# Kernel tuning notes

Measured on AMD Instinct MI355X. Metric: run time of the kernel, lower is better.

Reference implementation:

```python
import jax, jax.numpy as jnp
import numpy as np

WH, WW = 8, 8          # window_size
NUM_HEADS = 16
DIM = 512
NW = 64                # windows per image (mask leading dim)
BATCH = 16             # images
N = WH * WW            # tokens per window


def _relative_position_index():
    coords = np.stack(np.meshgrid(np.arange(WH), np.arange(WW), indexing='ij'))  # (2,Wh,Ww)
    cf = coords.reshape(2, -1)                                                   # (2,N)
    rel = cf[:, :, None] - cf[:, None, :]                                        # (2,N,N)
    rel = rel.transpose(1, 2, 0).astype(np.int64)                                # (N,N,2)
    rel[:, :, 0] += WH - 1
    rel[:, :, 1] += WW - 1
    rel[:, :, 0] *= 2 * WW - 1
    return jnp.asarray(rel.sum(-1), dtype=jnp.int32)                             # (N,N)


def setup_inputs() -> dict:
    key = jax.random.key(0)
    ks = jax.random.split(key, 8)
    B_ = BATCH * NW
    x = jax.random.normal(ks[0], (B_, N, DIM), dtype=jnp.float32)
    # 0 / -100 additive shift-style mask (Swin uses -100.0 for masked pairs)
    mraw = jax.random.uniform(ks[1], (NW, N, N))
    mask = jnp.where(mraw < 0.15, jnp.float32(-100.0), jnp.float32(0.0))
    qkv_w = jax.random.normal(ks[2], (3 * DIM, DIM), dtype=jnp.float32) * (DIM ** -0.5)
    qkv_b = jnp.zeros((3 * DIM,), dtype=jnp.float32)
    proj_w = jax.random.normal(ks[3], (DIM, DIM), dtype=jnp.float32) * (DIM ** -0.5)
    proj_b = jnp.zeros((DIM,), dtype=jnp.float32)
    n_rel = (2 * WH - 1) * (2 * WW - 1)  # 225
    rpb_table = jax.random.normal(ks[4], (n_rel, NUM_HEADS), dtype=jnp.float32) * 0.02
    rel_index = _relative_position_index()
    return {"x": x, "mask": mask, "qkv_w": qkv_w, "qkv_b": qkv_b,
            "proj_w": proj_w, "proj_b": proj_b, "rpb_table": rpb_table,
            "rel_index": rel_index}


def reference(x, mask, qkv_w, qkv_b, proj_w, proj_b, rpb_table, rel_index):
    B_, n, C = x.shape
    H = NUM_HEADS
    hd = C // H
    scale = hd ** -0.5
    qkv = x @ qkv_w.T + qkv_b                       # (B_, N, 3C)
    qkv = qkv.reshape(B_, n, 3, H, hd)
    q = qkv[:, :, 0].transpose(0, 2, 1, 3) * scale  # (B_, H, N, hd)
    k = qkv[:, :, 1].transpose(0, 2, 1, 3)
    v = qkv[:, :, 2].transpose(0, 2, 1, 3)
    attn = jnp.einsum('bhnd,bhmd->bhnm', q, k)      # (B_, H, N, N)
    bias = rpb_table[rel_index.reshape(-1)].reshape(n, n, H).transpose(2, 0, 1)  # (H,N,N)
    attn = attn + bias[None]
    nW = mask.shape[0]
    attn = attn.reshape(B_ // nW, nW, H, n, n) + mask[None, :, None]
    attn = jax.nn.softmax(attn.reshape(B_, H, n, n), axis=-1)
    out = jnp.einsum('bhnm,bhmd->bhnd', attn, v)    # (B_, H, N, hd)
    out = out.transpose(0, 2, 1, 3).reshape(B_, n, C)
    return out @ proj_w.T + proj_b
```

## Files before the change

### kernel.cpp

```cpp
#include <hip/hip_runtime.h>
#include <hip/hip_bf16.h>

typedef unsigned short u16;
typedef __attribute__((ext_vector_type(8))) short bfrag;
typedef __attribute__((ext_vector_type(4))) float ffrag;

#define NWIN_TOT 1024
#define NTOK 64
#define CDIM 512
#define NHEAD 16
#define HDIM 32
#define NW 64

__device__ __forceinline__ u16 f2bf(float f) {
  union { float f; unsigned u; } v; v.f = f;
  unsigned r = v.u + 0x7fffu + ((v.u >> 16) & 1u);
  return (u16)(r >> 16);
}

__device__ __forceinline__ float bfhi2f(unsigned hi_bits) {
  union { unsigned u; float f; } v; v.u = hi_bits; return v.f;
}

__device__ __forceinline__ ffrag mfma16(bfrag a, bfrag b, ffrag c) {
  return __builtin_amdgcn_mfma_f32_16x16x32_bf16(a, b, c, 0, 0, 0);
}

__device__ __forceinline__ void gload16(const u16* src, u16* lds) {
  __builtin_amdgcn_global_load_lds(
      (const __attribute__((address_space(1))) unsigned int*)src,
      (__attribute__((address_space(3))) unsigned int*)lds, 16, 0, 0);
}

#define BAR() __builtin_amdgcn_s_barrier()
#define VMW(n) do { asm volatile("s_waitcnt vmcnt(" #n ")" ::: "memory"); \
                    __builtin_amdgcn_sched_barrier(0); } while (0)

__global__ __launch_bounds__(256) void k_prep(const float* __restrict__ x,
                                              const float* __restrict__ qkv_w,
                                              const float* __restrict__ proj_w,
                                              const int*   __restrict__ rel_index,
                                              const float* __restrict__ rpb,
                                              const float* __restrict__ mask,
                                              u16* __restrict__ xb,
                                              u16* __restrict__ wq, u16* __restrict__ wp,
                                              u16* __restrict__ combB) {
  int i = blockIdx.x * 256 + threadIdx.x;
  if (i < 4194304) {
    int e = i * 8;
    const float4* xp = reinterpret_cast<const float4*>(x + e);
    float4 lo = xp[0], hi = xp[1];
    union { u16 u[8]; bfrag v; } pk;
    pk.u[0] = f2bf(lo.x); pk.u[1] = f2bf(lo.y); pk.u[2] = f2bf(lo.z); pk.u[3] = f2bf(lo.w);
    pk.u[4] = f2bf(hi.x); pk.u[5] = f2bf(hi.y); pk.u[6] = f2bf(hi.z); pk.u[7] = f2bf(hi.w);
    *reinterpret_cast<bfrag*>(xb + e) = pk.v;
    return;
  }
  i -= 4194304;
  if (i < 786432) { wq[i] = f2bf(qkv_w[i]); return; }
  i -= 786432;
  if (i < 262144) { wp[i] = f2bf(proj_w[i]); return; }
  i -= 262144;
  {
    int wh = i >> 12, rc = i & 4095;
    int w0 = wh >> 4, h = wh & 15;
    combB[i] = f2bf(rpb[rel_index[rc] * 16 + h] + mask[(w0 << 12) + rc]);
  }
}

template<int EPI>
__global__ __launch_bounds__(512, 1) void k_gemm3(const u16* __restrict__ A,
                                                  const u16* __restrict__ W,
                                                  const float* __restrict__ bias,
                                                  u16* __restrict__ qws, u16* __restrict__ kws,
                                                  u16* __restrict__ vws,
                                                  float* __restrict__ out) {
  constexpr int NT = (EPI == 0) ? 12 : 4;
  constexpr int NWG = 256 * NT;
  extern __shared__ __align__(16) u16 smem[];

  const int bid = blockIdx.x;
  const int tile = (bid & 7) * (NWG >> 3) + (bid >> 3);
  const int bn = tile % NT, bm = tile / NT;
  const int brow = bm << 8, bcol = bn << 7;

  const int tid = threadIdx.x;
  const int wv = tid >> 6, lane = tid & 63, c15 = lane & 15, g = lane >> 4;
  const int g4 = g * 4;
  const int wr = wv >> 1, wc = wv & 1;
  const ffrag zf = {0.f, 0.f, 0.f, 0.f};

  ffrag acc[4][4];
#pragma unroll
  for (int i = 0; i < 4; ++i)
#pragma unroll
    for (int n = 0; n < 4; ++n) acc[i][n] = zf;

  auto stageA = [&](int t) {
    u16* db = smem + (t % 3) * 24576;
#pragma unroll
    for (int l = 0; l < 4; ++l) {
      int e = l * 4096 + tid * 8;
      int r = e >> 6, cb = (e & 63) << 1;
      int scol = (cb ^ ((r & 7) << 4)) >> 1;
      gload16(A + (size_t)(brow + r) * 512 + t * 64 + scol, db + e);
    }
  };
  auto stageB = [&](int t) {
    u16* db = smem + (t % 3) * 24576 + 16384;
#pragma unroll
    for (int l = 0; l < 2; ++l) {
      int e = l * 4096 + tid * 8;
      int r = e >> 6, cb = (e & 63) << 1;
      int scol = (cb ^ ((r & 7) << 4)) >> 1;
      gload16(W + (size_t)(bcol + r) * 512 + t * 64 + scol, db + e);
    }
  };

  stageA(0); stageB(0); stageA(1); stageB(1);
  VMW(6);
  BAR();

  for (int t = 0; t < 8; ++t) {
    const char* As_ = (const char*)(smem + (t % 3) * 24576);
    const char* Bs_ = As_ + 32768;
    bfrag a_[4], b_[4];

#pragma unroll
    for (int i = 0; i < 4; ++i) {
      int ra = wr * 64 + i * 16 + c15;
      a_[i] = *(const bfrag*)(As_ + ra * 128 + ((g * 16) ^ ((ra & 7) << 4)));
    }
#pragma unroll
    for (int n = 0; n < 4; ++n) {
      int rb = wc * 64 + n * 16 + c15;
      b_[n] = *(const bfrag*)(Bs_ + rb * 128 + ((g * 16) ^ ((rb & 7) << 4)));
    }
    if (t + 2 < 8) stageA(t + 2);
    BAR();
    __builtin_amdgcn_s_setprio(1);
#pragma unroll
    for (int i = 0; i < 4; ++i)
#pragma unroll
      for (int n = 0; n < 4; ++n)
        acc[i][n] = mfma16(a_[i], b_[n], acc[i][n]);
    __builtin_amdgcn_s_setprio(0);

#pragma unroll
    for (int i = 0; i < 4; ++i) {
      int ra = wr * 64 + i * 16 + c15;
      a_[i] = *(const bfrag*)(As_ + ra * 128 + ((64 + g * 16) ^ ((ra & 7) << 4)));
    }
#pragma unroll
    for (int n = 0; n < 4; ++n) {
      int rb = wc * 64 + n * 16 + c15;
      b_[n] = *(const bfrag*)(Bs_ + rb * 128 + ((64 + g * 16) ^ ((rb & 7) << 4)));
    }
    if (t + 2 < 8) stageB(t + 2);
    __builtin_amdgcn_s_setprio(1);
#pragma unroll
    for (int i = 0; i < 4; ++i)
#pragma unroll
      for (int n = 0; n < 4; ++n)
        acc[i][n] = mfma16(a_[i], b_[n], acc[i][n]);
    __builtin_amdgcn_s_setprio(0);
    if (t < 6) { VMW(6); BAR(); }
    else if (t == 6) { VMW(0); BAR(); }
  }

  if (EPI == 0) {
    const float SCALE = 0.17677669529663687f;
    const int which = bn >> 2;
    const int win = (brow >> 6) + wr;
#pragma unroll
    for (int n = 0; n < 4; ++n) {
      int c = bcol + wc * 64 + n * 16 + c15;
      float bz = bias[c];
      int cq = c & 511, h = cq >> 5, d = cq & 31;
      size_t slab = ((size_t)(win * NHEAD + h)) << 11;
      if (which == 2) {
        u16* vp = vws + slab + (d << 6);
#pragma unroll
        for (int i = 0; i < 4; ++i) {
          int tok0 = i * 16 + g4;
          union { u16 u[4]; uint2 v; } pk;
#pragma unroll
          for (int r = 0; r < 4; ++r) pk.u[r] = f2bf(acc[i][n][r] + bz);
          *reinterpret_cast<uint2*>(vp + tok0) = pk.v;
        }
      } else {
        const float s = (which == 0) ? SCALE : 1.0f;
        u16* qp = ((which == 0) ? qws : kws) + slab + d;
#pragma unroll
        for (int i = 0; i < 4; ++i)
#pragma unroll
          for (int r = 0; r < 4; ++r)
            qp[(i * 16 + g4 + r) << 5] = f2bf((acc[i][n][r] + bz) * s);
      }
    }
  } else {
#pragma unroll
    for (int n = 0; n < 4; ++n) {
      int c = bcol + wc * 64 + n * 16 + c15;
      float bz = bias[c];
      float* po = out + (size_t)(brow + wr * 64) * CDIM + c;
#pragma unroll
      for (int i = 0; i < 4; ++i)
#pragma unroll
        for (int r = 0; r < 4; ++r)
          po[(size_t)(i * 16 + g4 + r) * CDIM] = acc[i][n][r] + bz;
    }
  }
}

__global__ __launch_bounds__(256) void k_attn(const u16* __restrict__ qws,
                                              const u16* __restrict__ kws,
                                              const u16* __restrict__ vws,
                                              const u16* __restrict__ combB,
                                              u16* __restrict__ yws) {
  __shared__ __align__(16) u16 plds[4][NTOK * NTOK];
  const int tid = threadIdx.x, w = tid >> 6, lane = tid & 63;
  const int c15 = lane & 15, g = lane >> 4, g4 = g * 4;
  const int p = blockIdx.x * 4 + w;
  const int b = p >> 4, h = p & 15;

  const u16* qb_ = qws + (size_t)p * (NTOK * HDIM);
  const u16* kb_ = kws + (size_t)p * (NTOK * HDIM);
  bfrag qa[4], ka[4];
#pragma unroll
  for (int t = 0; t < 4; ++t) {
    qa[t] = *reinterpret_cast<const bfrag*>(qb_ + (t * 16 + c15) * HDIM + g * 8);
    ka[t] = *reinterpret_cast<const bfrag*>(kb_ + (t * 16 + c15) * HDIM + g * 8);
  }

  const u16* cB = combB + ((size_t)(((b & (NW - 1)) << 4) + h) << 12);
  u16* pl = plds[w];
  const ffrag zf = {0.f, 0.f, 0.f, 0.f};

#pragma unroll
  for (int it = 0; it < 4; ++it) {
    int row = it * 16 + c15;
    float l[4][4];
    float mx = -3.0e38f;
#pragma unroll
    for (int jt = 0; jt < 4; ++jt) {
      ffrag s = mfma16(ka[jt], qa[it], zf);
      uint2 cw = *reinterpret_cast<const uint2*>(cB + row * 64 + jt * 16 + g4);
      l[jt][0] = s[0] + bfhi2f(cw.x << 16);
      l[jt][1] = s[1] + bfhi2f(cw.x & 0xffff0000u);
      l[jt][2] = s[2] + bfhi2f(cw.y << 16);
      l[jt][3] = s[3] + bfhi2f(cw.y & 0xffff0000u);
      mx = fmaxf(mx, fmaxf(fmaxf(l[jt][0], l[jt][1]), fmaxf(l[jt][2], l[jt][3])));
    }
    mx = fmaxf(mx, __shfl_xor(mx, 16));
    mx = fmaxf(mx, __shfl_xor(mx, 32));
    float sum = 0.f;
#pragma unroll
    for (int jt = 0; jt < 4; ++jt)
#pragma unroll
      for (int r = 0; r < 4; ++r) {
        float e = __expf(l[jt][r] - mx);
        l[jt][r] = e;
        sum += e;
      }
    sum += __shfl_xor(sum, 16);
    sum += __shfl_xor(sum, 32);
    float inv = 1.0f / sum;
#pragma unroll
    for (int jt = 0; jt < 4; ++jt) {
      union { u16 u[4]; uint2 v; } pk;
#pragma unroll
      for (int r = 0; r < 4; ++r) pk.u[r] = f2bf(l[jt][r] * inv);
      int off = row * 64 + ((jt * 16 + g4) ^ ((row & 7) << 3));
      *reinterpret_cast<uint2*>(&pl[off]) = pk.v;
    }
  }
  __syncthreads();

  const u16* vb_ = vws + (size_t)p * (HDIM * NTOK);
  ffrag o0[4] = {zf, zf, zf, zf}, o1[4] = {zf, zf, zf, zf};
#pragma unroll
  for (int ks = 0; ks < 2; ++ks) {
    bfrag vf0 = *reinterpret_cast<const bfrag*>(vb_ + c15 * NTOK + ks * 32 + g * 8);
    bfrag vf1 = *reinterpret_cast<const bfrag*>(vb_ + (16 + c15) * NTOK + ks * 32 + g * 8);
#pragma unroll
    for (int i = 0; i < 4; ++i) {
      int prow = i * 16 + c15;
      bfrag pa = *reinterpret_cast<const bfrag*>(
          &pl[prow * 64 + ((ks * 32 + g * 8) ^ ((prow & 7) << 3))]);
      o0[i] = mfma16(pa, vf0, o0[i]);
      o1[i] = mfma16(pa, vf1, o1[i]);
    }
  }
  __syncthreads();

  u16* yl = &plds[0][0];
#pragma unroll
  for (int i = 0; i < 4; ++i)
#pragma unroll
    for (int r = 0; r < 4; ++r) {
      int tok = i * 16 + g4 + r;
      yl[tok * 136 + w * 32 + c15] = f2bf(o0[i][r]);
      yl[tok * 136 + w * 32 + 16 + c15] = f2bf(o1[i][r]);
    }
  __syncthreads();
  {
    const int b2 = blockIdx.x >> 2;
    const int h0 = (blockIdx.x * 4) & 15;
    int row = tid >> 2, seg = tid & 3;
    const u16* src = yl + row * 136 + seg * 32;
    u16* dst = yws + ((size_t)b2 * NTOK + row) * CDIM + h0 * HDIM + seg * 32;
    bfrag v0 = *(const bfrag*)(src);
    bfrag v1 = *(const bfrag*)(src + 8);
    bfrag v2 = *(const bfrag*)(src + 16);
    bfrag v3 = *(const bfrag*)(src + 24);
    *(bfrag*)(dst) = v0;
    *(bfrag*)(dst + 8) = v1;
    *(bfrag*)(dst + 16) = v2;
    *(bfrag*)(dst + 24) = v3;
  }
}

extern "C" void kernel_launch(void* const* d_in, const int* in_sizes, int n_in,
                              void* d_out, int out_size, void* d_ws, size_t ws_size,
                              hipStream_t stream) {
  const float* x      = (const float*)d_in[0];
  const float* mask   = (const float*)d_in[1];
  const float* qkv_w  = (const float*)d_in[2];
  const float* qkv_b  = (const float*)d_in[3];
  const float* proj_w = (const float*)d_in[4];
  const float* proj_b = (const float*)d_in[5];
  const float* rpb    = (const float*)d_in[6];
  const int*   rel    = (const int*)d_in[7];
  float* out = (float*)d_out;

  char* ws = (char*)d_ws;
  constexpr size_t SZ_QKV = (size_t)NWIN_TOT * NHEAD * NTOK * HDIM * 2;
  u16* qws = (u16*)(ws);
  u16* kws = (u16*)(ws + SZ_QKV);
  u16* vws = (u16*)(ws + 2 * SZ_QKV);
  u16* xb  = (u16*)(ws + 3 * SZ_QKV);
  u16* yws = xb;
  u16* wq  = (u16*)(ws + 4 * SZ_QKV);
  u16* wp  = (u16*)(ws + 4 * SZ_QKV + 1572864);
  u16* combB = (u16*)(ws + 4 * SZ_QKV + 1572864 + 524288);

  hipFuncSetAttribute((const void*)k_gemm3<0>,
                      hipFuncAttributeMaxDynamicSharedMemorySize, 147456);
  hipFuncSetAttribute((const void*)k_gemm3<1>,
                      hipFuncAttributeMaxDynamicSharedMemorySize, 147456);

  k_prep<<<dim3(36864), dim3(256), 0, stream>>>(x, qkv_w, proj_w, rel, rpb, mask,
                                                xb, wq, wp, combB);
  k_gemm3<0><<<dim3(256 * 12), dim3(512), 147456, stream>>>(xb, wq, qkv_b,
                                                            qws, kws, vws, nullptr);
  k_attn<<<dim3(NWIN_TOT * NHEAD / 4), dim3(256), 0, stream>>>(qws, kws, vws, combB, yws);
  k_gemm3<1><<<dim3(256 * 4), dim3(512), 147456, stream>>>(yws, wp, proj_b,
                                                           nullptr, nullptr, nullptr, out);
}
```

Baseline: 324.5 us.

## Keep full 128-row A panel resident in LDS and stream weights from global

Restructures both GEMMs so each workgroup loads a 128x512 slab of activations into LDS once, then loops over all output column tiles, reading weight fragments straight from global memory (relying on cache) instead of staging them through LDS. The grid shrinks from thousands of 256x128 tiles to 512 row-panel workgroups, which removes the repeated re-reads of A across column tiles and the per-k-step barriers. In exchange it drops the triple-buffered software pipeline, uses a smaller per-wave accumulator tile, and makes the MFMA loop depend on global-load latency for W with no explicit prefetch.

New measurement: 417.3 us. 28.6% more time.

```diff
diff --git a/kernel.cpp b/kernel.cpp
--- a/kernel.cpp
+++ b/kernel.cpp
@@ -69,146 +69,111 @@
 }
 
 template<int EPI>
-__global__ __launch_bounds__(512, 1) void k_gemm3(const u16* __restrict__ A,
+__global__ __launch_bounds__(512, 1) void k_gemmA(const u16* __restrict__ A,
                                                   const u16* __restrict__ W,
                                                   const float* __restrict__ bias,
                                                   u16* __restrict__ qws, u16* __restrict__ kws,
                                                   u16* __restrict__ vws,
                                                   float* __restrict__ out) {
   constexpr int NT = (EPI == 0) ? 12 : 4;
-  constexpr int NWG = 256 * NT;
   extern __shared__ __align__(16) u16 smem[];
 
   const int bid = blockIdx.x;
-  const int tile = (bid & 7) * (NWG >> 3) + (bid >> 3);
-  const int bn = tile % NT, bm = tile / NT;
-  const int brow = bm << 8, bcol = bn << 7;
+  const int brow = bid << 7;
 
   const int tid = threadIdx.x;
   const int wv = tid >> 6, lane = tid & 63, c15 = lane & 15, g = lane >> 4;
   const int g4 = g * 4;
-  const int wr = wv >> 1, wc = wv & 1;
+  const int wr = wv >> 2, wc = wv & 3;
   const ffrag zf = {0.f, 0.f, 0.f, 0.f};
-
-  ffrag acc[4][4];
-#pragma unroll
-  for (int i = 0; i < 4; ++i)
-#pragma unroll
-    for (int n = 0; n < 4; ++n) acc[i][n] = zf;
-
-  auto stageA = [&](int t) {
-    u16* db = smem + (t % 3) * 24576;
-#pragma unroll
-    for (int l = 0; l < 4; ++l) {
-      int e = l * 4096 + tid * 8;
-      int r = e >> 6, cb = (e & 63) << 1;
-      int scol = (cb ^ ((r & 7) << 4)) >> 1;
-      gload16(A + (size_t)(brow + r) * 512 + t * 64 + scol, db + e);
-    }
-  };
-  auto stageB = [&](int t) {
-    u16* db = smem + (t % 3) * 24576 + 16384;
-#pragma unroll
-    for (int l = 0; l < 2; ++l) {
-      int e = l * 4096 + tid * 8;
-      int r = e >> 6, cb = (e & 63) << 1;
-      int scol = (cb ^ ((r & 7) << 4)) >> 1;
-      gload16(W + (size_t)(bcol + r) * 512 + t * 64 + scol, db + e);
-    }
-  };
-
-  stageA(0); stageB(0); stageA(1); stageB(1);
-  VMW(6);
+  const char* Asb = reinterpret_cast<const char*>(smem);
+
+#pragma unroll
+  for (int cl = 0; cl < 16; ++cl) {
+    int e = cl * 4096 + tid * 8;
+    int row = e >> 9, cb = (e & 511) << 1;
+    int scol = (cb ^ ((row & 7) << 4)) >> 1;
+    gload16(A + (size_t)(brow + row) * 512 + scol, smem + e);
+  }
+  VMW(0);
   BAR();
 
-  for (int t = 0; t < 8; ++t) {
-    const char* As_ = (const char*)(smem + (t % 3) * 24576);
-    const char* Bs_ = As_ + 32768;
-    bfrag a_[4], b_[4];
-
+  for (int nt = 0; nt < NT; ++nt) {
+    ffrag acc[4][2];
 #pragma unroll
     for (int i = 0; i < 4; ++i) {
-      int ra = wr * 64 + i * 16 + c15;
-      a_[i] = *(const bfrag*)(As_ + ra * 128 + ((g * 16) ^ ((ra & 7) << 4)));
-    }
-#pragma unroll
-    for (int n = 0; n < 4; ++n) {
-      int rb = wc * 64 + n * 16 + c15;
-      b_[n] = *(const bfrag*)(Bs_ + rb * 128 + ((g * 16) ^ ((rb & 7) << 4)));
-    }
-    if (t + 2 < 8) stageA(t + 2);
-    BAR();
-    __builtin_amdgcn_s_setprio(1);
-#pragma unroll
-    for (int i = 0; i < 4; ++i)
-#pragma unroll
-      for (int n = 0; n < 4; ++n)
-        acc[i][n] = mfma16(a_[i], b_[n], acc[i][n]);
-    __builtin_amdgcn_s_setprio(0);
-
-#pragma unroll
-    for (int i = 0; i < 4; ++i) {
-      int ra = wr * 64 + i * 16 + c15;
-      a_[i] = *(const bfrag*)(As_ + ra * 128 + ((64 + g * 16) ^ ((ra & 7) << 4)));
-    }
-#pragma unroll
-    for (int n = 0; n < 4; ++n) {
-      int rb = wc * 64 + n * 16 + c15;
-      b_[n] = *(const bfrag*)(Bs_ + rb * 128 + ((64 + g * 16) ^ ((rb & 7) << 4)));
-    }
-    if (t + 2 < 8) stageB(t + 2);
-    __builtin_amdgcn_s_setprio(1);
-#pragma unroll
-    for (int i = 0; i < 4; ++i)
-#pragma unroll
-      for (int n = 0; n < 4; ++n)
-        acc[i][n] = mfma16(a_[i], b_[n], acc[i][n]);
-    __builtin_amdgcn_s_setprio(0);
-    if (t < 6) { VMW(6); BAR(); }
-    else if (t == 6) { VMW(0); BAR(); }
-  }
-
-  if (EPI == 0) {
-    const float SCALE = 0.17677669529663687f;
-    const int which = bn >> 2;
-    const int win = (brow >> 6) + wr;
-#pragma unroll
-    for (int n = 0; n < 4; ++n) {
-      int c = bcol + wc * 64 + n * 16 + c15;
-      float bz = bias[c];
-      int cq = c & 511, h = cq >> 5, d = cq & 31;
-      size_t slab = ((size_t)(win * NHEAD + h)) << 11;
-      if (which == 2) {
-        u16* vp = vws + slab + (d << 6);
-#pragma unroll
-        for (int i = 0; i < 4; ++i) {
-          int tok0 = i * 16 + g4;
-          union { u16 u[4]; uint2 v; } pk;
-#pragma unroll
-          for (int r = 0; r < 4; ++r) pk.u[r] = f2bf(acc[i][n][r] + bz);
-          *reinterpret_cast<uint2*>(vp + tok0) = pk.v;
+      acc[i][0] = zf; acc[i][1] = zf;
+    }
+    const u16* Wn = W + (size_t)(nt * 128 + wc * 32) * 512;
+
+#pragma unroll 2
+    for (int t = 0; t < 8; ++t) {
+      bfrag a_[4][2], b_[2][2];
+#pragma unroll
+      for (int n = 0; n < 2; ++n)
+#pragma unroll
+        for (int ks = 0; ks < 2; ++ks)
+          b_[n][ks] = *reinterpret_cast<const bfrag*>(
+              Wn + (size_t)(n * 16 + c15) * 512 + t * 64 + ks * 32 + g * 8);
+#pragma unroll
+      for (int i = 0; i < 4; ++i) {
+        int ra = wr * 64 + i * 16 + c15;
+#pragma unroll
+        for (int ks = 0; ks < 2; ++ks)
+          a_[i][ks] = *reinterpret_cast<const bfrag*>(
+              Asb + ra * 1024 + ((t * 128 + ks * 64 + g * 16) ^ ((ra & 7) << 4)));
+      }
+#pragma unroll
+      for (int i = 0; i < 4; ++i)
+#pragma unroll
+        for (int n = 0; n < 2; ++n)
+#pragma unroll
+          for (int ks = 0; ks < 2; ++ks)
+            acc[i][n] = mfma16(a_[i][ks], b_[n][ks], acc[i][n]);
+    }
+
+    if (EPI == 0) {
+      const float SCALE = 0.17677669529663687f;
+      const int win = (brow >> 6) + wr;
+#pragma unroll
+      for (int n = 0; n < 2; ++n) {
+        int c = nt * 128 + wc * 32 + n * 16 + c15;
+        float bz = bias[c];
+        int which = c >> 9;
+        int cq = c & 511, h = cq >> 5, d = cq & 31;
+        size_t slab = ((size_t)(win * NHEAD + h)) << 11;
+        if (which == 2) {
+          u16* vp = vws + slab + (d << 6);
+#pragma unroll
+          for (int i = 0; i < 4; ++i) {
+            int tok0 = i * 16 + g4;
+            union { u16 u[4]; uint2 v; } pk;
+#pragma unroll
+            for (int r = 0; r < 4; ++r) pk.u[r] = f2bf(acc[i][n][r] + bz);
+            *reinterpret_cast<uint2*>(vp + tok0) = pk.v;
+          }
+        } else {
+          const float s2 = (which == 0) ? SCALE : 1.0f;
+          u16* qp = ((which == 0) ? qws : kws) + slab + d;
+#pragma unroll
+          for (int i = 0; i < 4; ++i)
+#pragma unroll
+            for (int r = 0; r < 4; ++r)
+              qp[(i * 16 + g4 + r) << 5] = f2bf((acc[i][n][r] + bz) * s2);
         }
-      } else {
-        const float s = (which == 0) ? SCALE : 1.0f;
-        u16* qp = ((which == 0) ? qws : kws) + slab + d;
+      }
+    } else {
+#pragma unroll
+      for (int n = 0; n < 2; ++n) {
+        int c = nt * 128 + wc * 32 + n * 16 + c15;
+        float bz = bias[c];
+        float* po = out + (size_t)(brow + wr * 64) * CDIM + c;
 #pragma unroll
         for (int i = 0; i < 4; ++i)
 #pragma unroll
           for (int r = 0; r < 4; ++r)
-            qp[(i * 16 + g4 + r) << 5] = f2bf((acc[i][n][r] + bz) * s);
+            po[(size_t)(i * 16 + g4 + r) * CDIM] = acc[i][n][r] + bz;
       }
-    }
-  } else {
-#pragma unroll
-    for (int n = 0; n < 4; ++n) {
-      int c = bcol + wc * 64 + n * 16 + c15;
-      float bz = bias[c];
-      float* po = out + (size_t)(brow + wr * 64) * CDIM + c;
-#pragma unroll
-      for (int i = 0; i < 4; ++i)
-#pragma unroll
-        for (int r = 0; r < 4; ++r)
-          po[(size_t)(i * 16 + g4 + r) * CDIM] = acc[i][n][r] + bz;
     }
   }
 }
@@ -345,16 +310,14 @@
   u16* wp  = (u16*)(ws + 4 * SZ_QKV + 1572864);
   u16* combB = (u16*)(ws + 4 * SZ_QKV + 1572864 + 524288);
 
-  hipFuncSetAttribute((const void*)k_gemm3<0>,
-                      hipFuncAttributeMaxDynamicSharedMemorySize, 147456);
-  hipFuncSetAttribute((const void*)k_gemm3<1>,
-                      hipFuncAttributeMaxDynamicSharedMemorySize, 147456);
+  hipFuncSetAttribute((const void*)k_gemmA<0>,
+                      hipFuncAttributeMaxDynamicSharedMemorySize, 131072);
+  hipFuncSetAttribute((const void*)k_gemmA<1>,
+                      hipFuncAttributeMaxDynamicSharedMemorySize, 131072);
 
   k_prep<<<dim3(36864), dim3(256), 0, stream>>>(x, qkv_w, proj_w, rel, rpb, mask,
                                                 xb, wq, wp, combB);
-  k_gemm3<0><<<dim3(256 * 12), dim3(512), 147456, stream>>>(xb, wq, qkv_b,
-                                                            qws, kws, vws, nullptr);
+  k_gemmA<0><<<dim3(512), dim3(512), 131072, stream>>>(xb, wq, qkv_b, qws, kws, vws, nullptr);
   k_attn<<<dim3(NWIN_TOT * NHEAD / 4), dim3(256), 0, stream>>>(qws, kws, vws, combB, yws);
-  k_gemm3<1><<<dim3(256 * 4), dim3(512), 147456, stream>>>(yws, wp, proj_b,
-                                                           nullptr, nullptr, nullptr, out);
-}
+  k_gemmA<1><<<dim3(512), dim3(512), 131072, stream>>>(yws, wp, proj_b, nullptr, nullptr, nullptr, out);
+}
```
